# Kernel tuning notes

Measured on AMD Instinct MI355X. Metric: run time of the kernel, lower is better.

Reference implementation:

```python
import jax, jax.numpy as jnp
import numpy as np

N = 50000      # cells (nodes)
E = 1600000    # directed edges (kNN connectivity graph)
F_IN = 2000    # highly-variable genes
HID = 16
H = 4          # GAT heads
C = 16         # GAT out channels per head
NUM_CLASSES = 3


def setup_inputs() -> dict:
    key = jax.random.key(0)
    ks = jax.random.split(key, 10)
    x = jax.random.normal(ks[0], (N, F_IN), dtype=jnp.float32)
    edge_index = jax.random.randint(ks[1], (2, E), 0, N, dtype=jnp.int64)
    s = 0.05
    W1 = jax.random.normal(ks[2], (F_IN, HID), dtype=jnp.float32) * s
    b1 = jnp.zeros((HID,), jnp.float32)
    Wg = jax.random.normal(ks[3], (HID, H * C), dtype=jnp.float32) * s
    att_src = jax.random.normal(ks[4], (H, C), dtype=jnp.float32) * s
    att_dst = jax.random.normal(ks[5], (H, C), dtype=jnp.float32) * s
    bg = jnp.zeros((H * C,), jnp.float32)
    Wo = jax.random.normal(ks[6], (H * C, NUM_CLASSES), dtype=jnp.float32) * s
    bo = jnp.zeros((NUM_CLASSES,), jnp.float32)
    return {"x": x, "edge_index": edge_index, "W1": W1, "b1": b1, "Wg": Wg,
            "att_src": att_src, "att_dst": att_dst, "bg": bg, "Wo": Wo, "bo": bo}


def reference(x, edge_index, W1, b1, Wg, att_src, att_dst, bg, Wo, bo):
    n = x.shape[0]
    loops = jnp.arange(n, dtype=edge_index.dtype)
    src = jnp.concatenate([edge_index[0], loops])  # [E+N]
    dst = jnp.concatenate([edge_index[1], loops])

    # ---- GCNConv(F_IN -> 16): project, symmetric-normalize, scatter-add ----
    h = x @ W1                                                   # [N, 16]
    deg = jax.ops.segment_sum(jnp.ones(src.shape, h.dtype), dst, num_segments=n)
    dinv = jnp.where(deg > 0, jax.lax.rsqrt(deg), 0.0)
    norm = dinv[src] * dinv[dst]                                 # [E+N]
    h = jax.ops.segment_sum(h[src] * norm[:, None], dst, num_segments=n) + b1
    h = jax.nn.relu(h)                                           # dropout is identity in eval

    # ---- GATConv(16 -> 16, heads=4, concat) ----
    g = (h @ Wg).reshape(n, H, C)                                # [N, H, C]
    a_s = jnp.einsum('nhc,hc->nh', g, att_src)                   # [N, H]
    a_d = jnp.einsum('nhc,hc->nh', g, att_dst)
    e = jax.nn.leaky_relu(a_s[src] + a_d[dst], 0.2)              # [E+N, H]
    m = jax.ops.segment_max(e, dst, num_segments=n)              # segment softmax (stable)
    ex = jnp.exp(e - m[dst])
    denom = jax.ops.segment_sum(ex, dst, num_segments=n)
    alpha = ex / (denom[dst] + 1e-16)                            # [E+N, H]
    out = jax.ops.segment_sum(g[src] * alpha[:, :, None], dst, num_segments=n)
    out = out.reshape(n, H * C) + bg                             # [N, 64]

    # ---- classifier head ----
    logits = out @ Wo + bo                                       # [N, 3]
    return jax.nn.log_softmax(logits, axis=1)
```

## Files before the change

### kernel.cpp

```cpp
#include <hip/hip_runtime.h>
#include <hip/hip_bf16.h>
#include <math.h>

#define F_IN   2000
#define HID    16
#define HEADS  4
#define CPH    16
#define HC     64
#define NCLS   3

__device__ __forceinline__ float lrelu(float x){ return x > 0.f ? x : 0.2f*x; }

__device__ __forceinline__ float comp4(const float4& v, int k){
  return k==0 ? v.x : k==1 ? v.y : k==2 ? v.z : v.w;
}

__device__ __forceinline__ float sel4(float a, float b, float c, float d, int h){
  float lo = (h&1) ? b : a;
  float hi = (h&1) ? d : c;
  return (h&2) ? hi : lo;
}

__global__ void k_zero(int* __restrict__ deg, int n) {
  int i = blockIdx.x * 256 + threadIdx.x;
  if (i < n) deg[i] = 0;
}

__global__ __launch_bounds__(256) void k_gemm1(const float* __restrict__ x,
                                               const float* __restrict__ W1,
                                               float* __restrict__ h0, int n) {
  __shared__ float w1s[8192];
  const int t    = threadIdx.x;
  const int lane = t & 63;
  const int wid  = t >> 6;
  const int rowbase = blockIdx.x * 16 + wid * 4;

  float acc[64];
  #pragma unroll
  for (int v = 0; v < 64; ++v) acc[v] = 0.f;

  for (int phase = 0; phase < 4; ++phase) {
    const int kbase = phase * 500;
    __syncthreads();
    #pragma unroll
    for (int k = 0; k < 8; ++k) {
      const int slotbase = (wid * 8 + k) * 64;
      const int slot = slotbase + lane;
      const int row_slot = slot >> 2;
      const int r = row_slot ^ ((row_slot >> 4) & 1);
      const int q = (slot & 3) ^ ((row_slot >> 2) & 3);
      int rg = kbase + r;
      if (rg > 1999) rg = 1999;
      __builtin_amdgcn_global_load_lds(
          (const __attribute__((address_space(1))) void*)(W1 + (size_t)rg * 16 + q * 4),
          (__attribute__((address_space(3))) void*)(w1s + (size_t)slotbase * 4),
          16, 0, 0);
    }
    __syncthreads();

    #pragma unroll
    for (int i = 0; i < 2; ++i) {
      int f4l = i * 64 + lane;
      if (f4l < 125) {
        float4 xv[4];
        #pragma unroll
        for (int r = 0; r < 4; ++r) {
          int row = rowbase + r;
          xv[r] = (row < n)
              ? *reinterpret_cast<const float4*>(
                    x + (size_t)row * F_IN + kbase + f4l * 4)
              : make_float4(0.f, 0.f, 0.f, 0.f);
        }
        const int qx = f4l & 3;
        const int xb = (f4l >> 2) & 1;
        #pragma unroll
        for (int kk = 0; kk < 4; ++kk) {
          const int rs = (4 * f4l + kk) ^ xb;
          const float* rowp = w1s + rs * 16;
          float xk0 = comp4(xv[0], kk), xk1 = comp4(xv[1], kk);
          float xk2 = comp4(xv[2], kk), xk3 = comp4(xv[3], kk);
          #pragma unroll
          for (int q = 0; q < 4; ++q) {
            float4 w4 = *reinterpret_cast<const float4*>(rowp + ((q ^ qx) << 2));
            acc[0*16+4*q+0] += xk0 * w4.x; acc[0*16+4*q+1] += xk0 * w4.y;
            acc[0*16+4*q+2] += xk0 * w4.z; acc[0*16+4*q+3] += xk0 * w4.w;
            acc[1*16+4*q+0] += xk1 * w4.x; acc[1*16+4*q+1] += xk1 * w4.y;
            acc[1*16+4*q+2] += xk1 * w4.z; acc[1*16+4*q+3] += xk1 * w4.w;
            acc[2*16+4*q+0] += xk2 * w4.x; acc[2*16+4*q+1] += xk2 * w4.y;
            acc[2*16+4*q+2] += xk2 * w4.z; acc[2*16+4*q+3] += xk2 * w4.w;
            acc[3*16+4*q+0] += xk3 * w4.x; acc[3*16+4*q+1] += xk3 * w4.y;
            acc[3*16+4*q+2] += xk3 * w4.z; acc[3*16+4*q+3] += xk3 * w4.w;
          }
        }
      }
    }
  }

  #pragma unroll
  for (int b = 32; b >= 1; b >>= 1) {
    bool hi = (lane & b) != 0;
    #pragma unroll
    for (int j = 0; j < b; ++j) {
      float send = hi ? acc[j] : acc[b + j];
      float recv = __shfl_xor(send, b);
      acc[j] = (hi ? acc[b + j] : acc[j]) + recv;
    }
  }
  int r = lane >> 4, c = lane & 15;
  int row = rowbase + r;
  if (row < n) h0[(size_t)row * 16 + c] = acc[0];
}

__global__ void k_deg(const int* __restrict__ edst, int* __restrict__ deg, int e) {
  int i = blockIdx.x * 256 + threadIdx.x;
  if (i < e) atomicAdd(&deg[edst[i]], 1);
}

__global__ void k_scan_a(const int* __restrict__ deg, int* __restrict__ bsum, int n) {
  __shared__ int s[256];
  int i = blockIdx.x * 256 + threadIdx.x;
  s[threadIdx.x] = (i < n) ? deg[i] : 0;
  __syncthreads();
  for (int off = 128; off > 0; off >>= 1) {
    if (threadIdx.x < off) s[threadIdx.x] += s[threadIdx.x + off];
    __syncthreads();
  }
  if (threadIdx.x == 0) bsum[blockIdx.x] = s[0];
}

__global__ void k_scan_b(int* __restrict__ bsum, int nb) {
  int lane = threadIdx.x;
  int carry = 0;
  for (int base = 0; base < nb; base += 64) {
    int idx = base + lane;
    int orig = (idx < nb) ? bsum[idx] : 0;
    int v = orig;
    #pragma unroll
    for (int off = 1; off < 64; off <<= 1) {
      int tv = __shfl_up(v, off);
      if (lane >= off) v += tv;
    }
    if (idx < nb) bsum[idx] = carry + v - orig;
    carry += __shfl(v, 63);
  }
}

__global__ void k_scan_c(const int* __restrict__ deg, const int* __restrict__ bsum,
                         int* __restrict__ rowptr, int* __restrict__ cursor,
                         float* __restrict__ dinv, int n) {
  __shared__ int s[256];
  int i = blockIdx.x * 256 + threadIdx.x;
  int v = (i < n) ? deg[i] : 0;
  s[threadIdx.x] = v;
  __syncthreads();
  for (int off = 1; off < 256; off <<= 1) {
    int tv = (threadIdx.x >= off) ? s[threadIdx.x - off] : 0;
    __syncthreads();
    s[threadIdx.x] += tv;
    __syncthreads();
  }
  int excl = s[threadIdx.x] - v + bsum[blockIdx.x];
  if (i < n) {
    rowptr[i] = excl;
    cursor[i] = excl;
    dinv[i] = rsqrtf((float)(v + 1));
    if (i == n - 1) rowptr[n] = excl + v;
  }
}

__global__ void k_scatter(const int* __restrict__ esrc, const int* __restrict__ edst,
                          int* __restrict__ cursor, int* __restrict__ csr, int e) {
  int i = blockIdx.x * 256 + threadIdx.x;
  if (i < e) {
    int d = edst[i];
    int pos = atomicAdd(&cursor[d], 1);
    csr[pos] = esrc[i];
  }
}

__global__ __launch_bounds__(256) void k_gcn(
    const float* __restrict__ h0, const int* __restrict__ rowptr,
    const int* __restrict__ csr, const float* __restrict__ dinv,
    const float* __restrict__ b1, const float* __restrict__ Wg,
    const float* __restrict__ atts, const float* __restrict__ attd,
    float* __restrict__ g, float* __restrict__ a_s, float* __restrict__ a_d, int n) {
  __shared__ float wgs[HID * HC];
  __shared__ float ats[HC], atd[HC];
  int t = threadIdx.x;
  for (int i = t; i < HID * HC; i += 256) wgs[i] = Wg[i];
  if (t < HC) { ats[t] = atts[t]; atd[t] = attd[t]; }
  __syncthreads();

  int lane = t & 63, w = t >> 6;
  int dst = blockIdx.x * 4 + w;
  if (dst >= n) return;
  int j = lane >> 4, c = lane & 15;
  int start = rowptr[dst], end = rowptr[dst + 1];
  float dd = dinv[dst];

  float acc = 0.f;
  for (int idx = start + j; idx < end; idx += 4) {
    int src = csr[idx];
    acc += h0[(size_t)src * 16 + c] * dinv[src];
  }
  acc += __shfl_xor(acc, 16);
  acc += __shfl_xor(acc, 32);
  acc = acc * dd + h0[(size_t)dst * 16 + c] * dd * dd;
  float hv = fmaxf(acc + b1[c], 0.f);

  float go = 0.f;
  #pragma unroll
  for (int k = 0; k < 16; ++k) {
    float hk = __shfl(hv, k);
    go += hk * wgs[k * HC + lane];
  }
  g[(size_t)dst * HC + lane] = go;

  float asv = go * ats[lane], adv = go * atd[lane];
  #pragma unroll
  for (int m = 1; m < 16; m <<= 1) {
    asv += __shfl_xor(asv, m);
    adv += __shfl_xor(adv, m);
  }
  if (c == 0) {
    a_s[(size_t)dst * 4 + j] = asv;
    a_d[(size_t)dst * 4 + j] = adv;
  }
}

__global__ __launch_bounds__(256) void k_gat(
    const float* __restrict__ g, const int* __restrict__ rowptr,
    const int* __restrict__ csr, const float* __restrict__ a_s,
    const float* __restrict__ a_d, const float* __restrict__ bg,
    const float* __restrict__ Wo, const float* __restrict__ bo,
    float* __restrict__ out, int n) {
  __shared__ float wos[HC * NCLS];
  __shared__ float bgs[HC];
  __shared__ float bos[NCLS];
  int t = threadIdx.x;
  if (t < HC * NCLS) wos[t] = Wo[t];
  if (t < HC) bgs[t] = bg[t];
  if (t < NCLS) bos[t] = bo[t];
  __syncthreads();

  int lane = t & 63, w = t >> 6;
  int dst = blockIdx.x * 4 + w;
  if (dst >= n) return;
  int start = rowptr[dst], end = rowptr[dst + 1];

  float4 ad4 = *reinterpret_cast<const float4*>(a_d + (size_t)dst * 4);
  float4 asS = *reinterpret_cast<const float4*>(a_s + (size_t)dst * 4);

  float m0 = -1e30f, m1 = -1e30f, m2 = -1e30f, m3 = -1e30f;
  for (int idx = start + lane; idx < end; idx += 64) {
    int src = csr[idx];
    float4 s4 = *reinterpret_cast<const float4*>(a_s + (size_t)src * 4);
    m0 = fmaxf(m0, lrelu(s4.x + ad4.x));
    m1 = fmaxf(m1, lrelu(s4.y + ad4.y));
    m2 = fmaxf(m2, lrelu(s4.z + ad4.z));
    m3 = fmaxf(m3, lrelu(s4.w + ad4.w));
  }
  #pragma unroll
  for (int msk = 32; msk >= 1; msk >>= 1) {
    m0 = fmaxf(m0, __shfl_xor(m0, msk));
    m1 = fmaxf(m1, __shfl_xor(m1, msk));
    m2 = fmaxf(m2, __shfl_xor(m2, msk));
    m3 = fmaxf(m3, __shfl_xor(m3, msk));
  }
  float es0 = lrelu(asS.x + ad4.x), es1 = lrelu(asS.y + ad4.y);
  float es2 = lrelu(asS.z + ad4.z), es3 = lrelu(asS.w + ad4.w);
  m0 = fmaxf(m0, es0); m1 = fmaxf(m1, es1);
  m2 = fmaxf(m2, es2); m3 = fmaxf(m3, es3);

  int j = lane >> 4, c = lane & 15, h = c >> 2;
  float mh  = sel4(m0, m1, m2, m3, h);
  float adh = sel4(ad4.x, ad4.y, ad4.z, ad4.w, h);
  float esh = sel4(es0, es1, es2, es3, h);

  float a0 = 0.f, a1 = 0.f, a2 = 0.f, a3 = 0.f, den = 0.f;
  for (int idx = start + j; idx < end; idx += 4) {
    int src = csr[idx];
    float e = lrelu(a_s[(size_t)src * 4 + h] + adh);
    float ex = __expf(e - mh);
    float4 gv = *reinterpret_cast<const float4*>(g + (size_t)src * HC + c * 4);
    a0 += ex * gv.x; a1 += ex * gv.y; a2 += ex * gv.z; a3 += ex * gv.w;
    den += ex;
  }
  if (j == 0) {
    float ex = __expf(esh - mh);
    float4 gv = *reinterpret_cast<const float4*>(g + (size_t)dst * HC + c * 4);
    a0 += ex * gv.x; a1 += ex * gv.y; a2 += ex * gv.z; a3 += ex * gv.w;
    den += ex;
  }
  a0 += __shfl_xor(a0, 16); a0 += __shfl_xor(a0, 32);
  a1 += __shfl_xor(a1, 16); a1 += __shfl_xor(a1, 32);
  a2 += __shfl_xor(a2, 16); a2 += __shfl_xor(a2, 32);
  a3 += __shfl_xor(a3, 16); a3 += __shfl_xor(a3, 32);
  den += __shfl_xor(den, 16); den += __shfl_xor(den, 32);
  den += 1e-16f;

  float o0 = a0 / den + bgs[c * 4 + 0];
  float o1 = a1 / den + bgs[c * 4 + 1];
  float o2 = a2 / den + bgs[c * 4 + 2];
  float o3 = a3 / den + bgs[c * 4 + 3];

  float p0 = 0.f, p1 = 0.f, p2 = 0.f;
  {
    int ch = c * 4;
    p0 += o0 * wos[(ch+0)*NCLS+0] + o1 * wos[(ch+1)*NCLS+0] + o2 * wos[(ch+2)*NCLS+0] + o3 * wos[(ch+3)*NCLS+0];
    p1 += o0 * wos[(ch+0)*NCLS+1] + o1 * wos[(ch+1)*NCLS+1] + o2 * wos[(ch+2)*NCLS+1] + o3 * wos[(ch+3)*NCLS+1];
    p2 += o0 * wos[(ch+0)*NCLS+2] + o1 * wos[(ch+1)*NCLS+2] + o2 * wos[(ch+2)*NCLS+2] + o3 * wos[(ch+3)*NCLS+2];
  }
  #pragma unroll
  for (int msk = 1; msk < 16; msk <<= 1) {
    p0 += __shfl_xor(p0, msk);
    p1 += __shfl_xor(p1, msk);
    p2 += __shfl_xor(p2, msk);
  }
  p0 += bos[0]; p1 += bos[1]; p2 += bos[2];
  float mx = fmaxf(p0, fmaxf(p1, p2));
  float ls = mx + logf(__expf(p0 - mx) + __expf(p1 - mx) + __expf(p2 - mx));
  if (lane == 0) {
    out[(size_t)dst * 3 + 0] = p0 - ls;
    out[(size_t)dst * 3 + 1] = p1 - ls;
    out[(size_t)dst * 3 + 2] = p2 - ls;
  }
}

extern "C" void kernel_launch(void* const* d_in, const int* in_sizes, int n_in,
                              void* d_out, int out_size, void* d_ws, size_t ws_size,
                              hipStream_t stream) {
  const float* x    = (const float*)d_in[0];
  const int*   ei   = (const int*)  d_in[1];
  const float* W1   = (const float*)d_in[2];
  const float* b1   = (const float*)d_in[3];
  const float* Wg   = (const float*)d_in[4];
  const float* atts = (const float*)d_in[5];
  const float* attd = (const float*)d_in[6];
  const float* bg   = (const float*)d_in[7];
  const float* Wo   = (const float*)d_in[8];
  const float* bo   = (const float*)d_in[9];
  float* out = (float*)d_out;

  const int n = in_sizes[0] / F_IN;
  const int e = in_sizes[1] / 2;
  const int* esrc = ei;
  const int* edst = ei + e;

  char* p = (char*)d_ws;
  auto alloc = [&](size_t bytes) { char* r = p; p += (bytes + 255) & ~(size_t)255; return r; };
  float* h0     = (float*)alloc((size_t)n * 16 * 4);
  int*   deg    = (int*)  alloc((size_t)n * 4);
  int*   cursor = (int*)  alloc((size_t)n * 4);
  float* dinv   = (float*)alloc((size_t)n * 4);
  int*   rowptr = (int*)  alloc((size_t)(n + 1) * 4);
  int*   bsum   = (int*)  alloc(4096);
  int*   csr    = (int*)  alloc((size_t)e * 4);
  float* gbuf   = (float*)alloc((size_t)n * HC * 4);
  float* as_    = (float*)alloc((size_t)n * 4 * 4);
  float* ad_    = (float*)alloc((size_t)n * 4 * 4);

  int nzb = (n + 255) / 256;
  k_zero<<<nzb, 256, 0, stream>>>(deg, n);

  k_gemm1<<<(n + 15) / 16, 256, 0, stream>>>(x, W1, h0, n);

  k_deg<<<(e + 255) / 256, 256, 0, stream>>>(edst, deg, e);

  int nb = (n + 255) / 256;
  k_scan_a<<<nb, 256, 0, stream>>>(deg, bsum, n);
  k_scan_b<<<1, 64, 0, stream>>>(bsum, nb);
  k_scan_c<<<nb, 256, 0, stream>>>(deg, bsum, rowptr, cursor, dinv, n);

  k_scatter<<<(e + 255) / 256, 256, 0, stream>>>(esrc, edst, cursor, csr, e);

  k_gcn<<<(n + 3) / 4, 256, 0, stream>>>(h0, rowptr, csr, dinv, b1, Wg, atts, attd,
                                         gbuf, as_, ad_, n);

  k_gat<<<(n + 3) / 4, 256, 0, stream>>>(gbuf, rowptr, csr, as_, ad_, bg, Wo, bo,
                                         out, n);
}
```

Before: 461.8 us.

## Store intermediates in bf16, double GEMM rows per wave with prefetch, use online softmax in GAT

Intermediate features h0 and g are stored as bf16, which halves the bytes moved by the random gathers in the GCN and GAT aggregation. The projection GEMM now computes 8 rows per wave with 128 accumulators and software-prefetches the next x chunk, for more W1 reuse and better latency hiding. The GAT kernel drops its separate max pass over edges and uses a single-pass online softmax merged across lanes. These trade precision for bandwidth and raise register pressure in the GEMM, which could cost occupancy.

```diff
diff --git a/kernel.cpp b/kernel.cpp
--- a/kernel.cpp
+++ b/kernel.cpp
@@ -15,10 +15,8 @@
   return k==0 ? v.x : k==1 ? v.y : k==2 ? v.z : v.w;
 }
 
-__device__ __forceinline__ float sel4(float a, float b, float c, float d, int h){
-  float lo = (h&1) ? b : a;
-  float hi = (h&1) ? d : c;
-  return (h&2) ? hi : lo;
+__device__ __forceinline__ float bf2f(unsigned short u){
+  return __uint_as_float(((unsigned)u) << 16);
 }
 
 __global__ void k_zero(int* __restrict__ deg, int n) {
@@ -26,22 +24,24 @@
   if (i < n) deg[i] = 0;
 }
 
-__global__ __launch_bounds__(256) void k_gemm1(const float* __restrict__ x,
-                                               const float* __restrict__ W1,
-                                               float* __restrict__ h0, int n) {
+__global__ __launch_bounds__(256, 2) void k_gemm1(const float* __restrict__ x,
+                                                  const float* __restrict__ W1,
+                                                  __hip_bfloat16* __restrict__ h0b,
+                                                  int n) {
   __shared__ float w1s[8192];
   const int t    = threadIdx.x;
   const int lane = t & 63;
   const int wid  = t >> 6;
-  const int rowbase = blockIdx.x * 16 + wid * 4;
-
-  float acc[64];
-  #pragma unroll
-  for (int v = 0; v < 64; ++v) acc[v] = 0.f;
-
-  for (int phase = 0; phase < 4; ++phase) {
+  const int rowbase = blockIdx.x * 32 + wid * 8;
+
+  float acc[128];
+  #pragma unroll
+  for (int v = 0; v < 128; ++v) acc[v] = 0.f;
+
+  float4 xc[8], xn[8];
+
+  auto stage = [&](int phase) {
     const int kbase = phase * 500;
-    __syncthreads();
     #pragma unroll
     for (int k = 0; k < 8; ++k) {
       const int slotbase = (wid * 8 + k) * 64;
@@ -56,43 +56,64 @@
           (__attribute__((address_space(3))) void*)(w1s + (size_t)slotbase * 4),
           16, 0, 0);
     }
-    __syncthreads();
-
+  };
+
+  auto loadx = [&](float4* xv, int c) {
+    const int i = c & 1;
+    const int f4l = i * 64 + lane;
+    const bool kv = (f4l < 125);
+    const int kb = (c >> 1) * 500 + f4l * 4;
     #pragma unroll
-    for (int i = 0; i < 2; ++i) {
-      int f4l = i * 64 + lane;
-      if (f4l < 125) {
-        float4 xv[4];
+    for (int r = 0; r < 8; ++r) {
+      int row = rowbase + r;
+      xv[r] = (kv && row < n)
+          ? *reinterpret_cast<const float4*>(x + (size_t)row * F_IN + kb)
+          : make_float4(0.f, 0.f, 0.f, 0.f);
+    }
+  };
+
+  auto compute = [&](const float4* xv, int c) {
+    const int i = c & 1;
+    const int f4l = i * 64 + lane;
+    const int qx = f4l & 3;
+    const int xb = (f4l >> 2) & 1;
+    #pragma unroll
+    for (int kk = 0; kk < 4; ++kk) {
+      const int rs = (4 * f4l + kk) ^ xb;
+      const float* rowp = w1s + rs * 16;
+      float xk[8];
+      #pragma unroll
+      for (int r = 0; r < 8; ++r) xk[r] = comp4(xv[r], kk);
+      #pragma unroll
+      for (int q = 0; q < 4; ++q) {
+        float4 w4 = *reinterpret_cast<const float4*>(rowp + ((q ^ qx) << 2));
         #pragma unroll
-        for (int r = 0; r < 4; ++r) {
-          int row = rowbase + r;
-          xv[r] = (row < n)
-              ? *reinterpret_cast<const float4*>(
-                    x + (size_t)row * F_IN + kbase + f4l * 4)
-              : make_float4(0.f, 0.f, 0.f, 0.f);
-        }
-        const int qx = f4l & 3;
-        const int xb = (f4l >> 2) & 1;
-        #pragma unroll
-        for (int kk = 0; kk < 4; ++kk) {
-          const int rs = (4 * f4l + kk) ^ xb;
-          const float* rowp = w1s + rs * 16;
-          float xk0 = comp4(xv[0], kk), xk1 = comp4(xv[1], kk);
-          float xk2 = comp4(xv[2], kk), xk3 = comp4(xv[3], kk);
-          #pragma unroll
-          for (int q = 0; q < 4; ++q) {
-            float4 w4 = *reinterpret_cast<const float4*>(rowp + ((q ^ qx) << 2));
-            acc[0*16+4*q+0] += xk0 * w4.x; acc[0*16+4*q+1] += xk0 * w4.y;
-            acc[0*16+4*q+2] += xk0 * w4.z; acc[0*16+4*q+3] += xk0 * w4.w;
-            acc[1*16+4*q+0] += xk1 * w4.x; acc[1*16+4*q+1] += xk1 * w4.y;
-            acc[1*16+4*q+2] += xk1 * w4.z; acc[1*16+4*q+3] += xk1 * w4.w;
-            acc[2*16+4*q+0] += xk2 * w4.x; acc[2*16+4*q+1] += xk2 * w4.y;
-            acc[2*16+4*q+2] += xk2 * w4.z; acc[2*16+4*q+3] += xk2 * w4.w;
-            acc[3*16+4*q+0] += xk3 * w4.x; acc[3*16+4*q+1] += xk3 * w4.y;
-            acc[3*16+4*q+2] += xk3 * w4.z; acc[3*16+4*q+3] += xk3 * w4.w;
-          }
+        for (int r = 0; r < 8; ++r) {
+          acc[r*16+4*q+0] += xk[r] * w4.x;
+          acc[r*16+4*q+1] += xk[r] * w4.y;
+          acc[r*16+4*q+2] += xk[r] * w4.z;
+          acc[r*16+4*q+3] += xk[r] * w4.w;
         }
       }
+    }
+  };
+
+  stage(0);
+  loadx(xc, 0);
+  __syncthreads();
+
+  #pragma unroll
+  for (int c = 0; c < 8; ++c) {
+    if (c < 7) loadx(xn, c + 1);
+    compute(xc, c);
+    if ((c & 1) == 1 && c < 7) {
+      __syncthreads();
+      stage((c >> 1) + 1);
+      __syncthreads();
+    }
+    if (c < 7) {
+      #pragma unroll
+      for (int r = 0; r < 8; ++r) xc[r] = xn[r];
     }
   }
 
@@ -101,14 +122,18 @@
     bool hi = (lane & b) != 0;
     #pragma unroll
     for (int j = 0; j < b; ++j) {
-      float send = hi ? acc[j] : acc[b + j];
-      float recv = __shfl_xor(send, b);
-      acc[j] = (hi ? acc[b + j] : acc[j]) + recv;
-    }
-  }
-  int r = lane >> 4, c = lane & 15;
-  int row = rowbase + r;
-  if (row < n) h0[(size_t)row * 16 + c] = acc[0];
+      float sA = hi ? acc[j] : acc[b + j];
+      float rA = __shfl_xor(sA, b);
+      acc[j] = (hi ? acc[b + j] : acc[j]) + rA;
+      float sB = hi ? acc[64 + j] : acc[64 + b + j];
+      float rB = __shfl_xor(sB, b);
+      acc[64 + j] = (hi ? acc[64 + b + j] : acc[64 + j]) + rB;
+    }
+  }
+  int r = lane >> 4, cch = lane & 15;
+  int row0 = rowbase + r, row1 = rowbase + 4 + r;
+  if (row0 < n) h0b[(size_t)row0 * 16 + cch] = __float2bfloat16(acc[0]);
+  if (row1 < n) h0b[(size_t)row1 * 16 + cch] = __float2bfloat16(acc[64]);
 }
 
 __global__ void k_deg(const int* __restrict__ edst, int* __restrict__ deg, int e) {
@@ -179,11 +204,12 @@
 }
 
 __global__ __launch_bounds__(256) void k_gcn(
-    const float* __restrict__ h0, const int* __restrict__ rowptr,
+    const unsigned short* __restrict__ h0b, const int* __restrict__ rowptr,
     const int* __restrict__ csr, const float* __restrict__ dinv,
     const float* __restrict__ b1, const float* __restrict__ Wg,
     const float* __restrict__ atts, const float* __restrict__ attd,
-    float* __restrict__ g, float* __restrict__ a_s, float* __restrict__ a_d, int n) {
+    __hip_bfloat16* __restrict__ gb, float* __restrict__ a_s,
+    float* __restrict__ a_d, int n) {
   __shared__ float wgs[HID * HC];
   __shared__ float ats[HC], atd[HC];
   int t = threadIdx.x;
@@ -201,11 +227,11 @@
   float acc = 0.f;
   for (int idx = start + j; idx < end; idx += 4) {
     int src = csr[idx];
-    acc += h0[(size_t)src * 16 + c] * dinv[src];
+    acc += bf2f(h0b[(size_t)src * 16 + c]) * dinv[src];
   }
   acc += __shfl_xor(acc, 16);
   acc += __shfl_xor(acc, 32);
-  acc = acc * dd + h0[(size_t)dst * 16 + c] * dd * dd;
+  acc = acc * dd + bf2f(h0b[(size_t)dst * 16 + c]) * dd * dd;
   float hv = fmaxf(acc + b1[c], 0.f);
 
   float go = 0.f;
@@ -214,7 +240,7 @@
     float hk = __shfl(hv, k);
     go += hk * wgs[k * HC + lane];
   }
-  g[(size_t)dst * HC + lane] = go;
+  gb[(size_t)dst * HC + lane] = __float2bfloat16(go);
 
   float asv = go * ats[lane], adv = go * atd[lane];
   #pragma unroll
@@ -229,7 +255,7 @@
 }
 
 __global__ __launch_bounds__(256) void k_gat(
-    const float* __restrict__ g, const int* __restrict__ rowptr,
+    const unsigned short* __restrict__ gb, const int* __restrict__ rowptr,
     const int* __restrict__ csr, const float* __restrict__ a_s,
     const float* __restrict__ a_d, const float* __restrict__ bg,
     const float* __restrict__ Wo, const float* __restrict__ bo,
@@ -247,56 +273,59 @@
   int dst = blockIdx.x * 4 + w;
   if (dst >= n) return;
   int start = rowptr[dst], end = rowptr[dst + 1];
-
-  float4 ad4 = *reinterpret_cast<const float4*>(a_d + (size_t)dst * 4);
-  float4 asS = *reinterpret_cast<const float4*>(a_s + (size_t)dst * 4);
-
-  float m0 = -1e30f, m1 = -1e30f, m2 = -1e30f, m3 = -1e30f;
-  for (int idx = start + lane; idx < end; idx += 64) {
-    int src = csr[idx];
-    float4 s4 = *reinterpret_cast<const float4*>(a_s + (size_t)src * 4);
-    m0 = fmaxf(m0, lrelu(s4.x + ad4.x));
-    m1 = fmaxf(m1, lrelu(s4.y + ad4.y));
-    m2 = fmaxf(m2, lrelu(s4.z + ad4.z));
-    m3 = fmaxf(m3, lrelu(s4.w + ad4.w));
-  }
-  #pragma unroll
-  for (int msk = 32; msk >= 1; msk >>= 1) {
-    m0 = fmaxf(m0, __shfl_xor(m0, msk));
-    m1 = fmaxf(m1, __shfl_xor(m1, msk));
-    m2 = fmaxf(m2, __shfl_xor(m2, msk));
-    m3 = fmaxf(m3, __shfl_xor(m3, msk));
-  }
-  float es0 = lrelu(asS.x + ad4.x), es1 = lrelu(asS.y + ad4.y);
-  float es2 = lrelu(asS.z + ad4.z), es3 = lrelu(asS.w + ad4.w);
-  m0 = fmaxf(m0, es0); m1 = fmaxf(m1, es1);
-  m2 = fmaxf(m2, es2); m3 = fmaxf(m3, es3);
-
   int j = lane >> 4, c = lane & 15, h = c >> 2;
-  float mh  = sel4(m0, m1, m2, m3, h);
-  float adh = sel4(ad4.x, ad4.y, ad4.z, ad4.w, h);
-  float esh = sel4(es0, es1, es2, es3, h);
-
-  float a0 = 0.f, a1 = 0.f, a2 = 0.f, a3 = 0.f, den = 0.f;
+
+  float adh = a_d[(size_t)dst * 4 + h];
+  float ash = a_s[(size_t)dst * 4 + h];
+
+  float m = -1e30f, den = 0.f;
+  float a0 = 0.f, a1 = 0.f, a2 = 0.f, a3 = 0.f;
+
   for (int idx = start + j; idx < end; idx += 4) {
     int src = csr[idx];
     float e = lrelu(a_s[(size_t)src * 4 + h] + adh);
-    float ex = __expf(e - mh);
-    float4 gv = *reinterpret_cast<const float4*>(g + (size_t)src * HC + c * 4);
-    a0 += ex * gv.x; a1 += ex * gv.y; a2 += ex * gv.z; a3 += ex * gv.w;
-    den += ex;
+    float mn = fmaxf(m, e);
+    float corr = __expf(m - mn);
+    float p = __expf(e - mn);
+    ushort4 u4 = *reinterpret_cast<const ushort4*>(gb + (size_t)src * HC + c * 4);
+    den = den * corr + p;
+    a0 = a0 * corr + p * bf2f(u4.x);
+    a1 = a1 * corr + p * bf2f(u4.y);
+    a2 = a2 * corr + p * bf2f(u4.z);
+    a3 = a3 * corr + p * bf2f(u4.w);
+    m = mn;
   }
   if (j == 0) {
-    float ex = __expf(esh - mh);
-    float4 gv = *reinterpret_cast<const float4*>(g + (size_t)dst * HC + c * 4);
-    a0 += ex * gv.x; a1 += ex * gv.y; a2 += ex * gv.z; a3 += ex * gv.w;
-    den += ex;
-  }
-  a0 += __shfl_xor(a0, 16); a0 += __shfl_xor(a0, 32);
-  a1 += __shfl_xor(a1, 16); a1 += __shfl_xor(a1, 32);
-  a2 += __shfl_xor(a2, 16); a2 += __shfl_xor(a2, 32);
-  a3 += __shfl_xor(a3, 16); a3 += __shfl_xor(a3, 32);
-  den += __shfl_xor(den, 16); den += __shfl_xor(den, 32);
+    float e = lrelu(ash + adh);
+    float mn = fmaxf(m, e);
+    float corr = __expf(m - mn);
+    float p = __expf(e - mn);
+    ushort4 u4 = *reinterpret_cast<const ushort4*>(gb + (size_t)dst * HC + c * 4);
+    den = den * corr + p;
+    a0 = a0 * corr + p * bf2f(u4.x);
+    a1 = a1 * corr + p * bf2f(u4.y);
+    a2 = a2 * corr + p * bf2f(u4.z);
+    a3 = a3 * corr + p * bf2f(u4.w);
+    m = mn;
+  }
+
+  #pragma unroll
+  for (int msk = 16; msk <= 32; msk <<= 1) {
+    float m2 = __shfl_xor(m, msk);
+    float d2 = __shfl_xor(den, msk);
+    float b0 = __shfl_xor(a0, msk);
+    float b1v = __shfl_xor(a1, msk);
+    float b2 = __shfl_xor(a2, msk);
+    float b3 = __shfl_xor(a3, msk);
+    float M = fmaxf(m, m2);
+    float c1 = __expf(m - M), c2 = __expf(m2 - M);
+    den = den * c1 + d2 * c2;
+    a0 = a0 * c1 + b0 * c2;
+    a1 = a1 * c1 + b1v * c2;
+    a2 = a2 * c1 + b2 * c2;
+    a3 = a3 * c1 + b3 * c2;
+    m = M;
+  }
   den += 1e-16f;
 
   float o0 = a0 / den + bgs[c * 4 + 0];
@@ -349,21 +378,21 @@
 
   char* p = (char*)d_ws;
   auto alloc = [&](size_t bytes) { char* r = p; p += (bytes + 255) & ~(size_t)255; return r; };
-  float* h0     = (float*)alloc((size_t)n * 16 * 4);
+  __hip_bfloat16* h0b = (__hip_bfloat16*)alloc((size_t)n * 16 * 2);
   int*   deg    = (int*)  alloc((size_t)n * 4);
   int*   cursor = (int*)  alloc((size_t)n * 4);
   float* dinv   = (float*)alloc((size_t)n * 4);
   int*   rowptr = (int*)  alloc((size_t)(n + 1) * 4);
   int*   bsum   = (int*)  alloc(4096);
   int*   csr    = (int*)  alloc((size_t)e * 4);
-  float* gbuf   = (float*)alloc((size_t)n * HC * 4);
+  __hip_bfloat16* gbuf = (__hip_bfloat16*)alloc((size_t)n * HC * 2);
   float* as_    = (float*)alloc((size_t)n * 4 * 4);
   float* ad_    = (float*)alloc((size_t)n * 4 * 4);
 
   int nzb = (n + 255) / 256;
   k_zero<<<nzb, 256, 0, stream>>>(deg, n);
 
-  k_gemm1<<<(n + 15) / 16, 256, 0, stream>>>(x, W1, h0, n);
+  k_gemm1<<<(n + 31) / 32, 256, 0, stream>>>(x, W1, h0b, n);
 
   k_deg<<<(e + 255) / 256, 256, 0, stream>>>(edst, deg, e);
 
@@ -374,9 +403,10 @@
 
   k_scatter<<<(e + 255) / 256, 256, 0, stream>>>(esrc, edst, cursor, csr, e);
 
-  k_gcn<<<(n + 3) / 4, 256, 0, stream>>>(h0, rowptr, csr, dinv, b1, Wg, atts, attd,
+  k_gcn<<<(n + 3) / 4, 256, 0, stream>>>((const unsigned short*)h0b, rowptr, csr,
+                                         dinv, b1, Wg, atts, attd,
                                          gbuf, as_, ad_, n);
 
-  k_gat<<<(n + 3) / 4, 256, 0, stream>>>(gbuf, rowptr, csr, as_, ad_, bg, Wo, bo,
-                                         out, n);
-}
+  k_gat<<<(n + 3) / 4, 256, 0, stream>>>((const unsigned short*)gbuf, rowptr, csr,
+                                         as_, ad_, bg, Wo, bo, out, n);
+}
```

Measured after the change: 981.1 us. 112% more time.
